# Kernel optimization log

Hardware: AMD Instinct MI355X
Metric: run time of the kernel (lower is better)

The kernel has to match this reference:

```python
import jax, jax.numpy as jnp
import numpy as np


def setup_inputs() -> dict:
    key = jax.random.key(0)
    k_z, k_cb = jax.random.split(key)
    B, S, D, K = 8, 4096, 256, 8192
    z = jax.random.normal(k_z, (B, S, D), dtype=jnp.float32)
    codebook = jax.random.normal(k_cb, (K, D), dtype=jnp.float32)
    return {"z": z, "codebook": codebook}


def reference(z, codebook):
    """BaseVectorQuantizer.get_quants with distance_type='square',
    padding_idx=-1 (disabled), prob_decay=0 (deterministic argmin).

    z: (B, S, D); codebook: (K, D).
    Returns (embedding (B, S, D), q_indices (B, S, 1)).

    Squared L2 distance uses the ||z||^2 + ||e||^2 - 2 z e^T expansion
    (same math as the broadcasted (z - e)^2 sum, but GEMM-based).
    """
    B, S, D = z.shape
    zf = z.reshape(-1, D)                               # (N, D), N = B*S
    z_sq = jnp.sum(zf * zf, axis=-1, keepdims=True)     # (N, 1)
    e_sq = jnp.sum(codebook * codebook, axis=-1)        # (K,)
    # (N, K) squared distances
    dist = z_sq + e_sq[None, :] - 2.0 * jnp.einsum("nd,kd->nk", zf, codebook)
    idx = jnp.argmin(dist, axis=1)                      # (N,)
    embedding = jnp.take(codebook, idx, axis=0).reshape(B, S, D)
    q_indices = idx.reshape(B, S, 1)
    return embedding, q_indices
```

## Files before the change

kernel.cpp:

```cpp
#include <hip/hip_runtime.h>

constexpr int D  = 256;
constexpr int K  = 8192;
constexpr int N  = 32768;

typedef _Float16 f16;
typedef f16   f16x8  __attribute__((ext_vector_type(8)));
typedef float f32x16 __attribute__((ext_vector_type(16)));

__device__ __forceinline__ void gload_lds16(const void* g, void* l) {
    __builtin_amdgcn_global_load_lds(
        (const __attribute__((address_space(1))) unsigned int*)g,
        (__attribute__((address_space(3))) unsigned int*)l,
        16, 0, 0);
}


__global__ void esq_kernel(const float* __restrict__ cb, float* __restrict__ esq) {
    const int lane = threadIdx.x & 63;
    const int code = (int)((blockIdx.x * (size_t)blockDim.x + threadIdx.x) >> 6);
    const float4 v = *reinterpret_cast<const float4*>(cb + (size_t)code * D + lane * 4);
    float s = v.x * v.x + v.y * v.y + v.z * v.z + v.w * v.w;
    #pragma unroll
    for (int m = 32; m >= 1; m >>= 1) s += __shfl_xor(s, m);
    if (lane == 0) esq[code] = s;
}

__global__ void cvt_t(const float* __restrict__ cb, f16* __restrict__ cbt) {
    const int g    = blockIdx.x * 256 + threadIdx.x;
    const int s    = g >> 13;
    const int code = g & 8191;
    const float* src = cb + (size_t)code * D + (s & 31) * 8;
    const float4 a  = *reinterpret_cast<const float4*>(src);
    const float4 b2 = *reinterpret_cast<const float4*>(src + 4);
    const float vf[8] = {a.x, a.y, a.z, a.w, b2.x, b2.y, b2.z, b2.w};
    f16x8 o;
    if (s < 32) {
        #pragma unroll
        for (int e = 0; e < 8; ++e) o[e] = (f16)vf[e];
    } else {
        #pragma unroll
        for (int e = 0; e < 8; ++e) {
            f16 h = (f16)vf[e];
            o[e] = (f16)((vf[e] - (float)h) * 1024.0f);
        }
    }
    *reinterpret_cast<f16x8*>(cbt + ((size_t)s * 8192 + code) * 8) = o;
}

__launch_bounds__(256, 1)
__global__ void vq32(const float* __restrict__ z, const f16* __restrict__ cbt,
                     const float* __restrict__ esq, const float* __restrict__ cb,
                     float* __restrict__ out) {
    __shared__ f16 buf[2][32768];

    const int tid  = threadIdx.x;
    const int w    = tid >> 6;
    const int l    = tid & 63;
    const int cid  = l & 31;
    const int half = l >> 5;
    const size_t wrow0 = (size_t)blockIdx.x * 128 + w * 32;

    f16x8 zh[16], zl[16];
    {
        const float* zr = z + (wrow0 + cid) * D + half * 8;
        #pragma unroll
        for (int u = 0; u < 16; ++u) {
            float4 a  = *reinterpret_cast<const float4*>(zr + u * 16);
            float4 b2 = *reinterpret_cast<const float4*>(zr + u * 16 + 4);
            float vf[8] = {a.x, a.y, a.z, a.w, b2.x, b2.y, b2.z, b2.w};
            f16x8 h, lo;
            #pragma unroll
            for (int e = 0; e < 8; ++e) {
                f16 hh = (f16)vf[e];
                h[e]  = hh;
                lo[e] = (f16)((vf[e] - (float)hh) * 1024.0f);
            }
            zh[u] = h; zl[u] = lo;
        }
    }

    float minv[16];
    int   mini[16];
    #pragma unroll
    for (int g = 0; g < 16; ++g) { minv[g] = 3.0e38f; mini[g] = 0; }

    f32x16 accA0 = (f32x16)0.0f, accA1 = (f32x16)0.0f;
    f32x16 accB0 = (f32x16)0.0f, accB1 = (f32x16)0.0f;

    {
        #pragma unroll
        for (int i = 0; i < 16; ++i) {
            const int s = w * 16 + i;
            gload_lds16(cbt + ((size_t)s * 8192 + l) * 8, &buf[0][(s * 64) * 8]);
        }
    }
    __syncthreads();

    for (int kt = 0; kt < 128; ++kt) {
        const int  b        = kt & 1;
        const bool haveNext = (kt < 127);

        if (haveNext) {
            const int k0n = (kt + 1) * 64;
            #pragma unroll
            for (int i = 0; i < 16; ++i) {
                const int s = w * 16 + i;
                gload_lds16(cbt + ((size_t)s * 8192 + k0n + l) * 8,
                            &buf[b ^ 1][(s * 64) * 8]);
            }
        }
        const float es0 = esq[kt * 64 + cid];
        const float es1 = esq[kt * 64 + 32 + cid];

        const f16* Bp = &buf[b][0];
        #pragma unroll
        for (int u = 0; u < 16; ++u) {
            f16x8 beh0 = *reinterpret_cast<const f16x8*>(Bp + ((2 * u + half) * 64 + cid) * 8);
            f16x8 beh1 = *reinterpret_cast<const f16x8*>(Bp + ((2 * u + half) * 64 + 32 + cid) * 8);
            f16x8 bel0 = *reinterpret_cast<const f16x8*>(Bp + ((32 + 2 * u + half) * 64 + cid) * 8);
            f16x8 bel1 = *reinterpret_cast<const f16x8*>(Bp + ((32 + 2 * u + half) * 64 + 32 + cid) * 8);
            accA0 = __builtin_amdgcn_mfma_f32_32x32x16_f16(zh[u], beh0, accA0, 0, 0, 0);
            accA1 = __builtin_amdgcn_mfma_f32_32x32x16_f16(zh[u], beh1, accA1, 0, 0, 0);
            accB0 = __builtin_amdgcn_mfma_f32_32x32x16_f16(zl[u], beh0, accB0, 0, 0, 0);
            accB1 = __builtin_amdgcn_mfma_f32_32x32x16_f16(zl[u], beh1, accB1, 0, 0, 0);
            accB0 = __builtin_amdgcn_mfma_f32_32x32x16_f16(zh[u], bel0, accB0, 0, 0, 0);
            accB1 = __builtin_amdgcn_mfma_f32_32x32x16_f16(zh[u], bel1, accB1, 0, 0, 0);
        }

        const int c0 = kt * 64 + cid;
        const int c1 = c0 + 32;
        #pragma unroll
        for (int g = 0; g < 16; ++g) {
            float d0 = fmaf(accB0[g], 0.0009765625f, accA0[g]);
            float s0 = fmaf(-2.0f, d0, es0);
            if (s0 < minv[g]) { minv[g] = s0; mini[g] = c0; }
            float d1 = fmaf(accB1[g], 0.0009765625f, accA1[g]);
            float s1 = fmaf(-2.0f, d1, es1);
            if (s1 < minv[g]) { minv[g] = s1; mini[g] = c1; }
        }
        accA0 = (f32x16)0.0f; accA1 = (f32x16)0.0f;
        accB0 = (f32x16)0.0f; accB1 = (f32x16)0.0f;

        if (haveNext) __syncthreads();
    }

    float* out_idx = out + (size_t)N * D;
    #pragma unroll
    for (int g = 0; g < 16; ++g) {
        float v   = minv[g];
        int   idx = mini[g];
        #pragma unroll
        for (int m = 1; m < 32; m <<= 1) {
            float ov = __shfl_xor(v, m);
            int   oi = __shfl_xor(idx, m);
            if (ov < v || (ov == v && oi < idx)) { v = ov; idx = oi; }
        }
        const size_t row = wrow0 + (g & 3) + 8 * (g >> 2) + 4 * half;
        if (cid == 0) out_idx[row] = (float)idx;
        const float4* src = reinterpret_cast<const float4*>(cb + (size_t)idx * D);
        float4*       dst = reinterpret_cast<float4*>(out + row * D);
        dst[cid]      = src[cid];
        dst[cid + 32] = src[cid + 32];
    }
}

constexpr int BM = 128, BN = 128, TD = 32, ZS = 260, CS = 36;

__launch_bounds__(256)
__global__ void vq_kernel(const float* __restrict__ z, const float* __restrict__ cb,
                          const float* __restrict__ esq, float* __restrict__ out) {
    __shared__ float zs[BM * ZS];
    __shared__ float cs[BN * CS];
    const int tid = threadIdx.x;
    const int tx  = tid & 15;
    const int ty  = tid >> 4;
    const size_t row0 = (size_t)blockIdx.x * BM;
    #pragma unroll
    for (int i = 0; i < 32; ++i) {
        int f  = tid + i * 256;
        int r  = f >> 6;
        int c4 = (f & 63) * 4;
        *reinterpret_cast<float4*>(&zs[r * ZS + c4]) =
            *reinterpret_cast<const float4*>(z + (row0 + r) * D + c4);
    }
    float minv[8]; int mini[8];
    #pragma unroll
    for (int i = 0; i < 8; ++i) { minv[i] = 3.4e38f; mini[i] = 0; }
    for (int k0 = 0; k0 < K; k0 += BN) {
        float acc[8][8];
        #pragma unroll
        for (int i = 0; i < 8; ++i)
            #pragma unroll
            for (int j = 0; j < 8; ++j) acc[i][j] = 0.0f;
        for (int dc = 0; dc < D; dc += TD) {
            __syncthreads();
            int c = tid >> 3, c4 = (tid & 7) * 4;
            #pragma unroll
            for (int i = 0; i < 4; ++i)
                *reinterpret_cast<float4*>(&cs[(c + 32 * i) * CS + c4]) =
                    *reinterpret_cast<const float4*>(cb + (size_t)(k0 + c + 32 * i) * D + dc + c4);
            __syncthreads();
            for (int d4 = 0; d4 < TD; d4 += 4) {
                float4 a[8], b[8];
                #pragma unroll
                for (int i = 0; i < 8; ++i)
                    a[i] = *reinterpret_cast<const float4*>(&zs[(ty + 16 * i) * ZS + dc + d4]);
                #pragma unroll
                for (int j = 0; j < 8; ++j)
                    b[j] = *reinterpret_cast<const float4*>(&cs[(tx + 16 * j) * CS + d4]);
                #pragma unroll
                for (int i = 0; i < 8; ++i)
                    #pragma unroll
                    for (int j = 0; j < 8; ++j)
                        acc[i][j] += a[i].x * b[j].x + a[i].y * b[j].y
                                   + a[i].z * b[j].z + a[i].w * b[j].w;
            }
        }
        #pragma unroll
        for (int j = 0; j < 8; ++j) {
            int code = k0 + tx + 16 * j;
            float es = esq[code];
            #pragma unroll
            for (int i = 0; i < 8; ++i) {
                float score = fmaf(-2.0f, acc[i][j], es);
                if (score < minv[i]) { minv[i] = score; mini[i] = code; }
            }
        }
    }
    float* out_idx = out + (size_t)N * D;
    #pragma unroll
    for (int i = 0; i < 8; ++i) {
        float v = minv[i]; int idx = mini[i];
        #pragma unroll
        for (int m = 1; m < 16; m <<= 1) {
            float ov = __shfl_xor(v, m);
            int   oi = __shfl_xor(idx, m);
            if (ov < v || (ov == v && oi < idx)) { v = ov; idx = oi; }
        }
        size_t row = row0 + ty + 16 * i;
        if (tx == 0) out_idx[row] = (float)idx;
        const float4* src = reinterpret_cast<const float4*>(cb + (size_t)idx * D);
        float4*       dst = reinterpret_cast<float4*>(out + row * D);
        #pragma unroll
        for (int t = 0; t < 4; ++t) dst[tx + 16 * t] = src[tx + 16 * t];
    }
}

extern "C" void kernel_launch(void* const* d_in, const int* in_sizes, int n_in,
                              void* d_out, int out_size, void* d_ws, size_t ws_size,
                              hipStream_t stream) {
    const float* z   = (const float*)d_in[0];
    const float* cb  = (const float*)d_in[1];
    float*       out = (float*)d_out;

    const size_t cbt_bytes = (size_t)K * 512 * sizeof(f16);
    const size_t need = cbt_bytes + (size_t)K * sizeof(float);

    if (ws_size >= need) {
        f16*   cbt  = (f16*)d_ws;
        float* esqp = (float*)((char*)d_ws + cbt_bytes);
        esq_kernel<<<(K * 64) / 256, 256, 0, stream>>>(cb, esqp);
        cvt_t<<<(K * 64) / 256, 256, 0, stream>>>(cb, cbt);
        vq32<<<N / 128, 256, 0, stream>>>(z, cbt, esqp, cb, out);
    } else {
        float* esqp = (float*)d_ws;
        esq_kernel<<<(K * 64) / 256, 256, 0, stream>>>(cb, esqp);
        vq_kernel<<<N / BM, 256, 0, stream>>>(z, cb, esqp, out);
    }
}
```

Before: 413.0 us.

## Split codebook across two blocks per row group and merge with gather kernel

Each 128-row group is now handled by two blocks, each scanning half the codebook with 32-code tiles. This halves LDS use and allows two blocks per CU, giving 512 blocks instead of 256. A new merge_gather kernel picks the better partial argmin and copies the codebook row. MFMA sections also get raised wave priority. The cost is redundant z loading and conversion per block, an extra kernel launch, and more workspace traffic. Ties between halves resolve to the first half, which keeps the lowest-index rule.

```diff
diff --git a/kernel.cpp b/kernel.cpp
--- a/kernel.cpp
+++ b/kernel.cpp
@@ -48,18 +48,21 @@
     *reinterpret_cast<f16x8*>(cbt + ((size_t)s * 8192 + code) * 8) = o;
 }
 
-__launch_bounds__(256, 1)
+__launch_bounds__(256, 2)
 __global__ void vq32(const float* __restrict__ z, const f16* __restrict__ cbt,
-                     const float* __restrict__ esq, const float* __restrict__ cb,
-                     float* __restrict__ out) {
-    __shared__ f16 buf[2][32768];
+                     const float* __restrict__ esq,
+                     float* __restrict__ wsv, int* __restrict__ wsi) {
+    __shared__ f16 buf[2][16384];
 
     const int tid  = threadIdx.x;
     const int w    = tid >> 6;
     const int l    = tid & 63;
     const int cid  = l & 31;
     const int half = l >> 5;
-    const size_t wrow0 = (size_t)blockIdx.x * 128 + w * 32;
+    const int rg    = blockIdx.x >> 1;
+    const int kh    = blockIdx.x & 1;
+    const int kbase = kh * 4096;
+    const size_t wrow0 = (size_t)rg * 128 + w * 32;
 
     f16x8 zh[16], zl[16];
     {
@@ -85,15 +88,13 @@
     #pragma unroll
     for (int g = 0; g < 16; ++g) { minv[g] = 3.0e38f; mini[g] = 0; }
 
-    f32x16 accA0 = (f32x16)0.0f, accA1 = (f32x16)0.0f;
-    f32x16 accB0 = (f32x16)0.0f, accB1 = (f32x16)0.0f;
-
-    {
-        #pragma unroll
-        for (int i = 0; i < 16; ++i) {
-            const int s = w * 16 + i;
-            gload_lds16(cbt + ((size_t)s * 8192 + l) * 8, &buf[0][(s * 64) * 8]);
-        }
+    f32x16 accA = (f32x16)0.0f, accB = (f32x16)0.0f;
+
+    #pragma unroll
+    for (int j = 0; j < 8; ++j) {
+        const int s = w * 16 + 2 * j + half;
+        gload_lds16(cbt + ((size_t)s * 8192 + kbase + cid) * 8,
+                    &buf[0][(w * 16 + 2 * j) * 256]);
     }
     __syncthreads();
 
@@ -102,50 +103,40 @@
         const bool haveNext = (kt < 127);
 
         if (haveNext) {
-            const int k0n = (kt + 1) * 64;
-            #pragma unroll
-            for (int i = 0; i < 16; ++i) {
-                const int s = w * 16 + i;
-                gload_lds16(cbt + ((size_t)s * 8192 + k0n + l) * 8,
-                            &buf[b ^ 1][(s * 64) * 8]);
-            }
-        }
-        const float es0 = esq[kt * 64 + cid];
-        const float es1 = esq[kt * 64 + 32 + cid];
+            const int k0n = kbase + (kt + 1) * 32;
+            #pragma unroll
+            for (int j = 0; j < 8; ++j) {
+                const int s = w * 16 + 2 * j + half;
+                gload_lds16(cbt + ((size_t)s * 8192 + k0n + cid) * 8,
+                            &buf[b ^ 1][(w * 16 + 2 * j) * 256]);
+            }
+        }
+        const float es = esq[kbase + kt * 32 + cid];
 
         const f16* Bp = &buf[b][0];
+        __builtin_amdgcn_s_setprio(1);
         #pragma unroll
         for (int u = 0; u < 16; ++u) {
-            f16x8 beh0 = *reinterpret_cast<const f16x8*>(Bp + ((2 * u + half) * 64 + cid) * 8);
-            f16x8 beh1 = *reinterpret_cast<const f16x8*>(Bp + ((2 * u + half) * 64 + 32 + cid) * 8);
-            f16x8 bel0 = *reinterpret_cast<const f16x8*>(Bp + ((32 + 2 * u + half) * 64 + cid) * 8);
-            f16x8 bel1 = *reinterpret_cast<const f16x8*>(Bp + ((32 + 2 * u + half) * 64 + 32 + cid) * 8);
-            accA0 = __builtin_amdgcn_mfma_f32_32x32x16_f16(zh[u], beh0, accA0, 0, 0, 0);
-            accA1 = __builtin_amdgcn_mfma_f32_32x32x16_f16(zh[u], beh1, accA1, 0, 0, 0);
-            accB0 = __builtin_amdgcn_mfma_f32_32x32x16_f16(zl[u], beh0, accB0, 0, 0, 0);
-            accB1 = __builtin_amdgcn_mfma_f32_32x32x16_f16(zl[u], beh1, accB1, 0, 0, 0);
-            accB0 = __builtin_amdgcn_mfma_f32_32x32x16_f16(zh[u], bel0, accB0, 0, 0, 0);
-            accB1 = __builtin_amdgcn_mfma_f32_32x32x16_f16(zh[u], bel1, accB1, 0, 0, 0);
-        }
-
-        const int c0 = kt * 64 + cid;
-        const int c1 = c0 + 32;
+            f16x8 beh = *reinterpret_cast<const f16x8*>(Bp + ((2 * u + half) * 32 + cid) * 8);
+            f16x8 bel = *reinterpret_cast<const f16x8*>(Bp + ((32 + 2 * u + half) * 32 + cid) * 8);
+            accA = __builtin_amdgcn_mfma_f32_32x32x16_f16(zh[u], beh, accA, 0, 0, 0);
+            accB = __builtin_amdgcn_mfma_f32_32x32x16_f16(zl[u], beh, accB, 0, 0, 0);
+            accB = __builtin_amdgcn_mfma_f32_32x32x16_f16(zh[u], bel, accB, 0, 0, 0);
+        }
+        __builtin_amdgcn_s_setprio(0);
+
+        const int c0 = kbase + kt * 32 + cid;
         #pragma unroll
         for (int g = 0; g < 16; ++g) {
-            float d0 = fmaf(accB0[g], 0.0009765625f, accA0[g]);
-            float s0 = fmaf(-2.0f, d0, es0);
-            if (s0 < minv[g]) { minv[g] = s0; mini[g] = c0; }
-            float d1 = fmaf(accB1[g], 0.0009765625f, accA1[g]);
-            float s1 = fmaf(-2.0f, d1, es1);
-            if (s1 < minv[g]) { minv[g] = s1; mini[g] = c1; }
-        }
-        accA0 = (f32x16)0.0f; accA1 = (f32x16)0.0f;
-        accB0 = (f32x16)0.0f; accB1 = (f32x16)0.0f;
+            float d = fmaf(accB[g], 0.0009765625f, accA[g]);
+            float s = fmaf(-2.0f, d, es);
+            if (s < minv[g]) { minv[g] = s; mini[g] = c0; }
+        }
+        accA = (f32x16)0.0f; accB = (f32x16)0.0f;
 
         if (haveNext) __syncthreads();
     }
 
-    float* out_idx = out + (size_t)N * D;
     #pragma unroll
     for (int g = 0; g < 16; ++g) {
         float v   = minv[g];
@@ -157,12 +148,26 @@
             if (ov < v || (ov == v && oi < idx)) { v = ov; idx = oi; }
         }
         const size_t row = wrow0 + (g & 3) + 8 * (g >> 2) + 4 * half;
-        if (cid == 0) out_idx[row] = (float)idx;
-        const float4* src = reinterpret_cast<const float4*>(cb + (size_t)idx * D);
-        float4*       dst = reinterpret_cast<float4*>(out + row * D);
-        dst[cid]      = src[cid];
-        dst[cid + 32] = src[cid + 32];
-    }
+        if (cid == 0) {
+            wsv[(size_t)kh * N + row] = v;
+            wsi[(size_t)kh * N + row] = idx;
+        }
+    }
+}
+
+__global__ void merge_gather(const float* __restrict__ wsv, const int* __restrict__ wsi,
+                             const float* __restrict__ cb, float* __restrict__ out) {
+    const int t   = threadIdx.x;
+    const int r   = blockIdx.x * 16 + (t >> 4);
+    const int l16 = t & 15;
+    const float v0 = wsv[r], v1 = wsv[N + r];
+    const int   i0 = wsi[r], i1 = wsi[N + r];
+    const int idx = (v1 < v0) ? i1 : i0;
+    if (l16 == 0) out[(size_t)N * D + r] = (float)idx;
+    const float4* src = reinterpret_cast<const float4*>(cb + (size_t)idx * D);
+    float4*       dst = reinterpret_cast<float4*>(out + (size_t)r * D);
+    #pragma unroll
+    for (int it = 0; it < 4; ++it) dst[l16 + 16 * it] = src[l16 + 16 * it];
 }
 
 constexpr int BM = 128, BN = 128, TD = 32, ZS = 260, CS = 36;
@@ -255,14 +260,21 @@
     float*       out = (float*)d_out;
 
     const size_t cbt_bytes = (size_t)K * 512 * sizeof(f16);
-    const size_t need = cbt_bytes + (size_t)K * sizeof(float);
+    const size_t esq_bytes = (size_t)K * sizeof(float);
+    const size_t wsv_bytes = (size_t)2 * N * sizeof(float);
+    const size_t wsi_bytes = (size_t)2 * N * sizeof(int);
+    const size_t need = cbt_bytes + esq_bytes + wsv_bytes + wsi_bytes;
 
     if (ws_size >= need) {
-        f16*   cbt  = (f16*)d_ws;
-        float* esqp = (float*)((char*)d_ws + cbt_bytes);
+        char* p = (char*)d_ws;
+        f16*   cbt  = (f16*)p;                 p += cbt_bytes;
+        float* esqp = (float*)p;               p += esq_bytes;
+        float* wsv  = (float*)p;               p += wsv_bytes;
+        int*   wsi  = (int*)p;
         esq_kernel<<<(K * 64) / 256, 256, 0, stream>>>(cb, esqp);
         cvt_t<<<(K * 64) / 256, 256, 0, stream>>>(cb, cbt);
-        vq32<<<N / 128, 256, 0, stream>>>(z, cbt, esqp, cb, out);
+        vq32<<<512, 256, 0, stream>>>(z, cbt, esqp, wsv, wsi);
+        merge_gather<<<N / 16, 256, 0, stream>>>(wsv, wsi, cb, out);
     } else {
         float* esqp = (float*)d_ws;
         esq_kernel<<<(K * 64) / 256, 256, 0, stream>>>(cb, esqp);
```

Result: faster. 368.9 us (-10.7%).
